# Optimization experiments

Hardware: AMD Instinct MI355X
Metric: run time of the kernel (lower is better)

Reference implementation:

```python
import jax, jax.numpy as jnp
import numpy as np

NUM_HEADS = 8
EPS = 1e-5


def setup_inputs() -> dict:
    key = jax.random.key(0)
    ks = jax.random.split(key, 12)
    B, S, D = 16384, 12, 512
    s = 1.0 / np.sqrt(D)
    return {
        "x": jax.random.normal(ks[0], (B, S, D), dtype=jnp.float32),
        "Wq": jax.random.uniform(ks[1], (D, D), jnp.float32, -s, s),
        "bq": jax.random.uniform(ks[2], (D,), jnp.float32, -s, s),
        "Wk": jax.random.uniform(ks[3], (D, D), jnp.float32, -s, s),
        "bk": jax.random.uniform(ks[4], (D,), jnp.float32, -s, s),
        "Wv": jax.random.uniform(ks[5], (D, D), jnp.float32, -s, s),
        "bv": jax.random.uniform(ks[6], (D,), jnp.float32, -s, s),
        "adj_bias": jnp.zeros((NUM_HEADS, S, S), dtype=jnp.float32),
        "Wo": jax.random.uniform(ks[7], (D, D), jnp.float32, -s, s),
        "bo": jax.random.uniform(ks[8], (D,), jnp.float32, -s, s),
        "gamma": jnp.ones((D,), dtype=jnp.float32),
        "beta": jnp.zeros((D,), dtype=jnp.float32),
    }


def reference(x, Wq, bq, Wk, bk, Wv, bv, adj_bias, Wo, bo, gamma, beta):
    B, S, D = x.shape
    H = NUM_HEADS
    hd = D // H
    # QKV projections -> (B, H, S, hd)
    def proj(W, b):
        return (jnp.einsum('bsd,de->bse', x, W) + b).reshape(B, S, H, hd).transpose(0, 2, 1, 3)
    q = proj(Wq, bq)
    k = proj(Wk, bk)
    v = proj(Wv, bv)
    # scores with learned adjacency bias: (B, H, S, S)
    scores = jnp.einsum('bhsd,bhtd->bhst', q, k) / np.sqrt(hd).astype(np.float32)
    scores = scores + adj_bias[None, :, :S, :S]
    attn = jax.nn.softmax(scores, axis=-1)  # dropout is identity in eval mode
    out = jnp.einsum('bhst,bhtd->bhsd', attn, v)
    out = out.transpose(0, 2, 1, 3).reshape(B, S, D)
    out = jnp.einsum('bsd,de->bse', out, Wo) + bo
    # residual (in_dim == out_dim) + LayerNorm
    y = out + x
    mu = jnp.mean(y, axis=-1, keepdims=True)
    var = jnp.mean(jnp.square(y - mu), axis=-1, keepdims=True)
    return (y - mu) * jax.lax.rsqrt(var + EPS) * gamma + beta
```

## Files before the change

kernel.cpp:

```cpp
#include <hip/hip_runtime.h>
#include <hip/hip_bf16.h>

#define D_DIM 512
#define S_LEN 12
#define H_NUM 8
#define WMAT 262144

#define G_B1 8
#define ROWS1 96
#define THREADS1 768
#define X_OFF   0
#define Q_OFF   98304
#define K_OFF   110592
#define V_OFF   122880
#define P_OFF   135168
#define SMEM1   142848

#define G_B2 8
#define ROWS2 96
#define THREADS2 512
#define AST_OFF 0
#define RED_OFF 98304
#define MU_OFF  104832
#define SMEM2   105600


typedef __attribute__((ext_vector_type(8))) short bf16x8;
typedef __attribute__((ext_vector_type(4))) float f32x4;

__device__ __forceinline__ unsigned short f2bf(float f) {
    union { float f; unsigned u; } c; c.f = f;
    unsigned r = c.u + 0x7fffu + ((c.u >> 16) & 1u);
    return (unsigned short)(r >> 16);
}
__device__ __forceinline__ float bf2f(unsigned short u) {
    union { unsigned u; float f; } c; c.u = ((unsigned)u) << 16;
    return c.f;
}
__device__ __forceinline__ int xswc(int row, int col) {
    return row * 512 + (((col >> 3) ^ (row & 7)) << 3) + (col & 7);
}
__device__ __forceinline__ int qsw(int row, int col) {
    return row * 64 + (((col >> 3) ^ (row & 7)) << 3) + (col & 7);
}

__global__ void prep_weights(const float* __restrict__ Wq, const float* __restrict__ Wk,
                             const float* __restrict__ Wv, const float* __restrict__ Wo,
                             unsigned short* __restrict__ wt) {
    int idx = blockIdx.x * 256 + threadIdx.x;
    int mat = idx >> 18;
    int rem = idx & (WMAT - 1);
    int e = rem >> 9, d = rem & 511;
    const float* W = (mat == 0) ? Wq : (mat == 1) ? Wk : (mat == 2) ? Wv : Wo;
    wt[idx] = f2bf(W[d * D_DIM + e]);
}

__global__ __launch_bounds__(THREADS1, 3) void qkv_attn(
    const float* __restrict__ x, const unsigned short* __restrict__ wt,
    const float* __restrict__ bq, const float* __restrict__ bk, const float* __restrict__ bv,
    const float* __restrict__ adj, unsigned short* __restrict__ aout)
{
    extern __shared__ char smem[];
    unsigned short* Xh = (unsigned short*)(smem + X_OFF);
    unsigned short* Qh = (unsigned short*)(smem + Q_OFF);
    unsigned short* Kh = (unsigned short*)(smem + K_OFF);
    unsigned short* Vh = (unsigned short*)(smem + V_OFF);
    float* Pl = (float*)(smem + P_OFF);

    const int tid  = threadIdx.x;
    const int lane = tid & 63;
    const int w    = tid >> 6;
    const int lr   = lane & 15;
    const int lg   = lane >> 4;
    const int lr12 = (lr < 12) ? lr : 11;
    const size_t row0 = (size_t)blockIdx.x * ROWS1;

    #pragma unroll
    for (int it = 0; it < 16; ++it) {
        int idx = it * THREADS1 + tid;
        int r = idx >> 7, col = (idx & 127) << 2;
        float4 v = *(const float4*)(x + (row0 + r) * (size_t)D_DIM + col);
        ushort4 pk;
        pk.x = f2bf(v.x); pk.y = f2bf(v.y); pk.z = f2bf(v.z); pk.w = f2bf(v.w);
        *(ushort4*)(Xh + xswc(r, col)) = pk;
    }
    __syncthreads();

    const int mat  = w >> 2;
    const int colt = w & 3;
    const int colh = colt * 16 + lr;
    const float* bsel = (mat == 0) ? bq : (mat == 1) ? bk : bv;
    unsigned short* T = (mat == 0) ? Qh : (mat == 1) ? Kh : Vh;
    const int rb = w * S_LEN;

    #pragma unroll 1
    for (int h = 0; h < H_NUM; ++h) {
        f32x4 acc[6];
        #pragma unroll
        for (int mt = 0; mt < 6; ++mt) acc[mt] = (f32x4){0.f, 0.f, 0.f, 0.f};

        const unsigned short* bAp = wt + (size_t)mat * WMAT + (h * 64 + colh) * D_DIM + lg * 8;
        bf16x8 bc = *(const bf16x8*)(bAp);
        #pragma unroll
        for (int ks = 0; ks < 16; ++ks) {
            bf16x8 bn;
            if (ks < 15) bn = *(const bf16x8*)(bAp + (ks + 1) * 32);
            #pragma unroll
            for (int mt = 0; mt < 6; ++mt) {
                bf16x8 af = *(const bf16x8*)(Xh + xswc(mt * 16 + lr, ks * 32 + lg * 8));
                acc[mt] = __builtin_amdgcn_mfma_f32_16x16x32_bf16(af, bc, acc[mt], 0, 0, 0);
            }
            if (ks < 15) bc = bn;
        }
        {
            float bias = bsel[h * 64 + colh];
            #pragma unroll
            for (int mt = 0; mt < 6; ++mt)
                #pragma unroll
                for (int j = 0; j < 4; ++j)
                    T[qsw(mt * 16 + lg * 4 + j, colh)] = f2bf(acc[mt][j] + bias);
        }
        __syncthreads();

        if (w < 8) {
            f32x4 sacc = (f32x4){0.f, 0.f, 0.f, 0.f};
            #pragma unroll
            for (int k2 = 0; k2 < 2; ++k2) {
                bf16x8 ak = *(const bf16x8*)(Kh + qsw(rb + lr12, k2 * 32 + lg * 8));
                bf16x8 aq = *(const bf16x8*)(Qh + qsw(rb + lr12, k2 * 32 + lg * 8));
                sacc = __builtin_amdgcn_mfma_f32_16x16x32_bf16(ak, aq, sacc, 0, 0, 0);
            }
            float ab4[4] = {0.f, 0.f, 0.f, 0.f};
            if (lg < 3 && lr < 12) {
                float4 t4 = *(const float4*)(adj + (h * S_LEN + lr) * S_LEN + lg * 4);
                ab4[0] = t4.x; ab4[1] = t4.y; ab4[2] = t4.z; ab4[3] = t4.w;
            }
            float sc[4], e4[4];
            float m = -1e30f;
            #pragma unroll
            for (int j = 0; j < 4; ++j) {
                int t = lg * 4 + j;
                sc[j] = (t < 12) ? (sacc[j] * 0.125f + ab4[j]) : -1e30f;
                m = fmaxf(m, sc[j]);
            }
            m = fmaxf(m, __shfl_xor(m, 16));
            m = fmaxf(m, __shfl_xor(m, 32));
            float ssum = 0.f;
            #pragma unroll
            for (int j = 0; j < 4; ++j) { e4[j] = __expf(sc[j] - m); ssum += e4[j]; }
            ssum += __shfl_xor(ssum, 16);
            ssum += __shfl_xor(ssum, 32);
            float inv = 1.f / ssum;
            float* Pw = Pl + w * 240;
            if (lr < 12 && lg < 3) {
                f32x4 pvec = (f32x4){e4[0] * inv, e4[1] * inv, e4[2] * inv, e4[3] * inv};
                *(f32x4*)(Pw + lr * 20 + lg * 4) = pvec;
            }
            float vv[12];
            #pragma unroll
            for (int t = 0; t < 12; ++t) vv[t] = bf2f(Vh[qsw(rb + t, lane)]);
            #pragma unroll
            for (int ss = 0; ss < 12; ++ss) {
                f32x4 pa = *(const f32x4*)(Pw + ss * 20);
                f32x4 pb = *(const f32x4*)(Pw + ss * 20 + 4);
                f32x4 pc = *(const f32x4*)(Pw + ss * 20 + 8);
                float o = 0.f;
                #pragma unroll
                for (int t = 0; t < 4; ++t) o += pa[t] * vv[t];
                #pragma unroll
                for (int t = 0; t < 4; ++t) o += pb[t] * vv[4 + t];
                #pragma unroll
                for (int t = 0; t < 4; ++t) o += pc[t] * vv[8 + t];
                aout[(row0 + rb + ss) * 1024 + h * 64 + lane] = f2bf(o);
            }
        }
        __syncthreads();
    }
}

__global__ __launch_bounds__(THREADS2, 2) void oproj_ln(
    const float* __restrict__ x, const unsigned short* __restrict__ wt,
    const float* __restrict__ bo, const float* __restrict__ gamma,
    const float* __restrict__ beta, float* __restrict__ out)
{
    extern __shared__ char smem[];
    unsigned short* Ast = (unsigned short*)(smem + AST_OFF);
    float* red   = (float*)(smem + RED_OFF);
    float* musig = (float*)(smem + MU_OFF);

    const int tid  = threadIdx.x;
    const int lane = tid & 63;
    const int w    = tid >> 6;
    const int lr   = lane & 15;
    const int lg   = lane >> 4;
    const size_t row0 = (size_t)blockIdx.x * ROWS2;
    const unsigned short* abase = (const unsigned short*)out;

    #pragma unroll
    for (int it = 0; it < 12; ++it) {
        int idx = it * THREADS2 + tid;
        int r = idx >> 6, c8 = (idx & 63) << 3;
        uint4 v = *(const uint4*)(abase + (row0 + r) * 1024 + c8);
        *(uint4*)(Ast + xswc(r, c8)) = v;
    }
    __syncthreads();

    f32x4 Y[6][4];
    #pragma unroll
    for (int mt = 0; mt < 6; ++mt)
        #pragma unroll
        for (int nt = 0; nt < 4; ++nt) Y[mt][nt] = (f32x4){0.f, 0.f, 0.f, 0.f};

    const unsigned short* obase = wt + (size_t)3 * WMAT + (w * 64 + lr) * D_DIM;
    #pragma unroll 1
    for (int ks = 0; ks < 16; ++ks) {
        bf16x8 afr[6];
        #pragma unroll
        for (int mt = 0; mt < 6; ++mt)
            afr[mt] = *(const bf16x8*)(Ast + xswc(mt * 16 + lr, ks * 32 + lg * 8));
        #pragma unroll
        for (int nt = 0; nt < 4; ++nt) {
            bf16x8 bfr = *(const bf16x8*)(obase + nt * 16 * D_DIM + ks * 32 + lg * 8);
            #pragma unroll
            for (int mt = 0; mt < 6; ++mt)
                Y[mt][nt] = __builtin_amdgcn_mfma_f32_16x16x32_bf16(afr[mt], bfr, Y[mt][nt], 0, 0, 0);
        }
    }

    float bo4[4], gm4[4], bt4[4];
    int cols[4];
    #pragma unroll
    for (int nt = 0; nt < 4; ++nt) {
        cols[nt] = w * 64 + nt * 16 + lr;
        bo4[nt] = bo[cols[nt]]; gm4[nt] = gamma[cols[nt]]; bt4[nt] = beta[cols[nt]];
    }
    #pragma unroll
    for (int mt = 0; mt < 6; ++mt)
        #pragma unroll
        for (int j = 0; j < 4; ++j) {
            int rowl = mt * 16 + lg * 4 + j;
            const float* xrow = x + (row0 + rowl) * (size_t)D_DIM;
            float ps = 0.f, pq = 0.f;
            #pragma unroll
            for (int nt = 0; nt < 4; ++nt) {
                float y = Y[mt][nt][j] + bo4[nt] + xrow[cols[nt]];
                Y[mt][nt][j] = y;
                ps += y; pq += y * y;
            }
            ps += __shfl_xor(ps, 1); pq += __shfl_xor(pq, 1);
            ps += __shfl_xor(ps, 2); pq += __shfl_xor(pq, 2);
            ps += __shfl_xor(ps, 4); pq += __shfl_xor(pq, 4);
            ps += __shfl_xor(ps, 8); pq += __shfl_xor(pq, 8);
            if (lr == 0) { red[rowl * 17 + w * 2] = ps; red[rowl * 17 + w * 2 + 1] = pq; }
        }
    __syncthreads();
    if (tid < ROWS2) {
        float s = 0.f, q = 0.f;
        #pragma unroll
        for (int w8 = 0; w8 < 8; ++w8) { s += red[tid * 17 + w8 * 2]; q += red[tid * 17 + w8 * 2 + 1]; }
        float mu = s * (1.f / 512.f);
        float var = q * (1.f / 512.f) - mu * mu;
        musig[tid * 2] = mu;
        musig[tid * 2 + 1] = rsqrtf(var + 1e-5f);
    }
    __syncthreads();
    #pragma unroll
    for (int mt = 0; mt < 6; ++mt)
        #pragma unroll
        for (int j = 0; j < 4; ++j) {
            int rowl = mt * 16 + lg * 4 + j;
            float mu = musig[rowl * 2], rs = musig[rowl * 2 + 1];
            float* orow = out + (row0 + rowl) * (size_t)D_DIM;
            #pragma unroll
            for (int nt = 0; nt < 4; ++nt)
                orow[cols[nt]] = (Y[mt][nt][j] - mu) * rs * gm4[nt] + bt4[nt];
        }
}

extern "C" void kernel_launch(void* const* d_in, const int* in_sizes, int n_in,
                              void* d_out, int out_size, void* d_ws, size_t ws_size,
                              hipStream_t stream) {
    (void)in_sizes; (void)n_in; (void)out_size; (void)ws_size;
    const float* x     = (const float*)d_in[0];
    const float* Wq    = (const float*)d_in[1];
    const float* bq    = (const float*)d_in[2];
    const float* Wk    = (const float*)d_in[3];
    const float* bk    = (const float*)d_in[4];
    const float* Wv    = (const float*)d_in[5];
    const float* bv    = (const float*)d_in[6];
    const float* adj   = (const float*)d_in[7];
    const float* Wo    = (const float*)d_in[8];
    const float* bo    = (const float*)d_in[9];
    const float* gamma = (const float*)d_in[10];
    const float* beta  = (const float*)d_in[11];
    unsigned short* wt = (unsigned short*)d_ws;

    prep_weights<<<4096, 256, 0, stream>>>(Wq, Wk, Wv, Wo, wt);
    qkv_attn<<<16384 / G_B1, THREADS1, SMEM1, stream>>>(
        x, wt, bq, bk, bv, adj, (unsigned short*)d_out);
    oproj_ln<<<16384 / G_B2, THREADS2, SMEM2, stream>>>(
        x, wt, bo, gamma, beta, (float*)d_out);
}
```

Before: 943.4 us.

## Stream x in double-buffered K-chunks and process two heads per pass

Instead of staging the whole 96x512 bf16 x tile in LDS once, the QKV kernel now streams x in 128-column chunks through a double buffer and computes two heads per pass. This re-reads x from global four times rather than once. Each A fragment loaded from LDS now feeds two MFMAs, and attention work is spread over 16 items across all 12 warps. The LDS footprint is smaller, but the chunk staging adds extra global traffic, more barriers per pass, and twice the accumulator registers.

```diff
diff --git a/kernel.cpp b/kernel.cpp
--- a/kernel.cpp
+++ b/kernel.cpp
@@ -9,12 +9,14 @@
 #define G_B1 8
 #define ROWS1 96
 #define THREADS1 768
-#define X_OFF   0
-#define Q_OFF   98304
-#define K_OFF   110592
-#define V_OFF   122880
-#define P_OFF   135168
-#define SMEM1   142848
+#define TBLK    6144
+#define XC_OFF  0
+#define XCB     24576
+#define Q_OFF   49152
+#define K_OFF   73728
+#define V_OFF   98304
+#define P_OFF   122880
+#define SMEM1   138240
 
 #define G_B2 8
 #define ROWS2 96
@@ -39,6 +41,9 @@
 }
 __device__ __forceinline__ int xswc(int row, int col) {
     return row * 512 + (((col >> 3) ^ (row & 7)) << 3) + (col & 7);
+}
+__device__ __forceinline__ int xcs(int row, int col) {
+    return row * 128 + (((col >> 3) ^ (row & 7)) << 3) + (col & 7);
 }
 __device__ __forceinline__ int qsw(int row, int col) {
     return row * 64 + (((col >> 3) ^ (row & 7)) << 3) + (col & 7);
@@ -61,7 +66,7 @@
     const float* __restrict__ adj, unsigned short* __restrict__ aout)
 {
     extern __shared__ char smem[];
-    unsigned short* Xh = (unsigned short*)(smem + X_OFF);
+    unsigned short* Xc = (unsigned short*)(smem + XC_OFF);
     unsigned short* Qh = (unsigned short*)(smem + Q_OFF);
     unsigned short* Kh = (unsigned short*)(smem + K_OFF);
     unsigned short* Vh = (unsigned short*)(smem + V_OFF);
@@ -75,59 +80,85 @@
     const int lr12 = (lr < 12) ? lr : 11;
     const size_t row0 = (size_t)blockIdx.x * ROWS1;
 
-    #pragma unroll
-    for (int it = 0; it < 16; ++it) {
-        int idx = it * THREADS1 + tid;
-        int r = idx >> 7, col = (idx & 127) << 2;
-        float4 v = *(const float4*)(x + (row0 + r) * (size_t)D_DIM + col);
-        ushort4 pk;
-        pk.x = f2bf(v.x); pk.y = f2bf(v.y); pk.z = f2bf(v.z); pk.w = f2bf(v.w);
-        *(ushort4*)(Xh + xswc(r, col)) = pk;
-    }
-    __syncthreads();
-
     const int mat  = w >> 2;
     const int colt = w & 3;
     const int colh = colt * 16 + lr;
     const float* bsel = (mat == 0) ? bq : (mat == 1) ? bk : bv;
-    unsigned short* T = (mat == 0) ? Qh : (mat == 1) ? Kh : Vh;
-    const int rb = w * S_LEN;
+    unsigned short* Tbase = (mat == 0) ? Qh : (mat == 1) ? Kh : Vh;
+
+#define STAGE_CHUNK(c)                                                          \
+    {                                                                           \
+        unsigned short* dst = Xc + ((c) & 1) * (XCB / 2);                       \
+        _Pragma("unroll")                                                       \
+        for (int it = 0; it < 4; ++it) {                                        \
+            int idx = it * THREADS1 + tid;                                      \
+            int r = idx >> 5, col = (idx & 31) << 2;                            \
+            float4 v = *(const float4*)(x + (row0 + r) * (size_t)D_DIM + (c) * 128 + col); \
+            ushort4 pk;                                                         \
+            pk.x = f2bf(v.x); pk.y = f2bf(v.y); pk.z = f2bf(v.z); pk.w = f2bf(v.w); \
+            *(ushort4*)(dst + xcs(r, col)) = pk;                                \
+        }                                                                       \
+    }
 
     #pragma unroll 1
-    for (int h = 0; h < H_NUM; ++h) {
-        f32x4 acc[6];
-        #pragma unroll
-        for (int mt = 0; mt < 6; ++mt) acc[mt] = (f32x4){0.f, 0.f, 0.f, 0.f};
-
-        const unsigned short* bAp = wt + (size_t)mat * WMAT + (h * 64 + colh) * D_DIM + lg * 8;
-        bf16x8 bc = *(const bf16x8*)(bAp);
-        #pragma unroll
-        for (int ks = 0; ks < 16; ++ks) {
-            bf16x8 bn;
-            if (ks < 15) bn = *(const bf16x8*)(bAp + (ks + 1) * 32);
-            #pragma unroll
-            for (int mt = 0; mt < 6; ++mt) {
-                bf16x8 af = *(const bf16x8*)(Xh + xswc(mt * 16 + lr, ks * 32 + lg * 8));
-                acc[mt] = __builtin_amdgcn_mfma_f32_16x16x32_bf16(af, bc, acc[mt], 0, 0, 0);
-            }
-            if (ks < 15) bc = bn;
+    for (int ep = 0; ep < 4; ++ep) {
+        const int h0 = ep * 2, h1 = ep * 2 + 1;
+        f32x4 accA[6], accB[6];
+        #pragma unroll
+        for (int mt = 0; mt < 6; ++mt) {
+            accA[mt] = (f32x4){0.f, 0.f, 0.f, 0.f};
+            accB[mt] = (f32x4){0.f, 0.f, 0.f, 0.f};
+        }
+        const unsigned short* b0base = wt + (size_t)mat * WMAT + (h0 * 64 + colh) * D_DIM + lg * 8;
+        const unsigned short* b1base = wt + (size_t)mat * WMAT + (h1 * 64 + colh) * D_DIM + lg * 8;
+
+        STAGE_CHUNK(0)
+        __syncthreads();
+        #pragma unroll
+        for (int c = 0; c < 4; ++c) {
+            if (c < 3) STAGE_CHUNK(c + 1)
+            const unsigned short* Xb = Xc + (c & 1) * (XCB / 2);
+            #pragma unroll
+            for (int kk = 0; kk < 4; ++kk) {
+                bf16x8 b0 = *(const bf16x8*)(b0base + c * 128 + kk * 32);
+                bf16x8 b1 = *(const bf16x8*)(b1base + c * 128 + kk * 32);
+                #pragma unroll
+                for (int mt = 0; mt < 6; ++mt) {
+                    bf16x8 af = *(const bf16x8*)(Xb + xcs(mt * 16 + lr, kk * 32 + lg * 8));
+                    accA[mt] = __builtin_amdgcn_mfma_f32_16x16x32_bf16(af, b0, accA[mt], 0, 0, 0);
+                    accB[mt] = __builtin_amdgcn_mfma_f32_16x16x32_bf16(af, b1, accB[mt], 0, 0, 0);
+                }
+            }
+            __syncthreads();
         }
         {
-            float bias = bsel[h * 64 + colh];
+            float bias0 = bsel[h0 * 64 + colh];
+            float bias1 = bsel[h1 * 64 + colh];
             #pragma unroll
             for (int mt = 0; mt < 6; ++mt)
                 #pragma unroll
-                for (int j = 0; j < 4; ++j)
-                    T[qsw(mt * 16 + lg * 4 + j, colh)] = f2bf(acc[mt][j] + bias);
+                for (int j = 0; j < 4; ++j) {
+                    int rowl = mt * 16 + lg * 4 + j;
+                    Tbase[qsw(rowl, colh)]        = f2bf(accA[mt][j] + bias0);
+                    Tbase[TBLK + qsw(rowl, colh)] = f2bf(accB[mt][j] + bias1);
+                }
         }
         __syncthreads();
 
-        if (w < 8) {
+        for (int t = w; t < 16; t += 12) {
+            const int item = t & 7;
+            const int hh2  = t >> 3;
+            const int h    = ep * 2 + hh2;
+            const int rbA  = item * S_LEN;
+            const unsigned short* Qb = Qh + hh2 * TBLK;
+            const unsigned short* Kb = Kh + hh2 * TBLK;
+            const unsigned short* Vb = Vh + hh2 * TBLK;
+
             f32x4 sacc = (f32x4){0.f, 0.f, 0.f, 0.f};
             #pragma unroll
             for (int k2 = 0; k2 < 2; ++k2) {
-                bf16x8 ak = *(const bf16x8*)(Kh + qsw(rb + lr12, k2 * 32 + lg * 8));
-                bf16x8 aq = *(const bf16x8*)(Qh + qsw(rb + lr12, k2 * 32 + lg * 8));
+                bf16x8 ak = *(const bf16x8*)(Kb + qsw(rbA + lr12, k2 * 32 + lg * 8));
+                bf16x8 aq = *(const bf16x8*)(Qb + qsw(rbA + lr12, k2 * 32 + lg * 8));
                 sacc = __builtin_amdgcn_mfma_f32_16x16x32_bf16(ak, aq, sacc, 0, 0, 0);
             }
             float ab4[4] = {0.f, 0.f, 0.f, 0.f};
@@ -139,8 +170,8 @@
             float m = -1e30f;
             #pragma unroll
             for (int j = 0; j < 4; ++j) {
-                int t = lg * 4 + j;
-                sc[j] = (t < 12) ? (sacc[j] * 0.125f + ab4[j]) : -1e30f;
+                int tt = lg * 4 + j;
+                sc[j] = (tt < 12) ? (sacc[j] * 0.125f + ab4[j]) : -1e30f;
                 m = fmaxf(m, sc[j]);
             }
             m = fmaxf(m, __shfl_xor(m, 16));
@@ -151,14 +182,14 @@
             ssum += __shfl_xor(ssum, 16);
             ssum += __shfl_xor(ssum, 32);
             float inv = 1.f / ssum;
-            float* Pw = Pl + w * 240;
+            float* Pw = Pl + t * 240;
             if (lr < 12 && lg < 3) {
                 f32x4 pvec = (f32x4){e4[0] * inv, e4[1] * inv, e4[2] * inv, e4[3] * inv};
                 *(f32x4*)(Pw + lr * 20 + lg * 4) = pvec;
             }
             float vv[12];
             #pragma unroll
-            for (int t = 0; t < 12; ++t) vv[t] = bf2f(Vh[qsw(rb + t, lane)]);
+            for (int t2 = 0; t2 < 12; ++t2) vv[t2] = bf2f(Vb[qsw(rbA + t2, lane)]);
             #pragma unroll
             for (int ss = 0; ss < 12; ++ss) {
                 f32x4 pa = *(const f32x4*)(Pw + ss * 20);
@@ -166,16 +197,17 @@
                 f32x4 pc = *(const f32x4*)(Pw + ss * 20 + 8);
                 float o = 0.f;
                 #pragma unroll
-                for (int t = 0; t < 4; ++t) o += pa[t] * vv[t];
-                #pragma unroll
-                for (int t = 0; t < 4; ++t) o += pb[t] * vv[4 + t];
-                #pragma unroll
-                for (int t = 0; t < 4; ++t) o += pc[t] * vv[8 + t];
-                aout[(row0 + rb + ss) * 1024 + h * 64 + lane] = f2bf(o);
+                for (int t2 = 0; t2 < 4; ++t2) o += pa[t2] * vv[t2];
+                #pragma unroll
+                for (int t2 = 0; t2 < 4; ++t2) o += pb[t2] * vv[4 + t2];
+                #pragma unroll
+                for (int t2 = 0; t2 < 4; ++t2) o += pc[t2] * vv[8 + t2];
+                aout[(row0 + rbA + ss) * 1024 + h * 64 + lane] = f2bf(o);
             }
         }
         __syncthreads();
     }
+#undef STAGE_CHUNK
 }
 
 __global__ __launch_bounds__(THREADS2, 2) void oproj_ln(
```

Result: slower. 1.013 ms (+7.4%).
